# Optimization experiments

Hardware: AMD Instinct MI355X
Metric: run time of the kernel (lower is better)

The kernel has to match this reference:

```python
import jax, jax.numpy as jnp
import numpy as np

B, C_IN, C_OUT, H, W = 128, 128, 128, 40, 40
NUM_EXPERTS, TOP_K, EXPAND = 8, 2, 2
C_HID = C_IN * EXPAND


def setup_inputs() -> dict:
    key = jax.random.key(0)
    ks = jax.random.split(key, 6)
    x = jax.random.normal(ks[0], (B, C_IN, H, W), dtype=jnp.float32)
    weights = jax.random.uniform(ks[1], (B, TOP_K), dtype=jnp.float32)
    indices = jax.random.randint(ks[2], (B, TOP_K), 0, NUM_EXPERTS, dtype=jnp.int64)
    # per-expert 1x1 conv params: expand -> SiLU -> project
    W1 = jax.random.normal(ks[3], (NUM_EXPERTS, C_HID, C_IN), dtype=jnp.float32) * (1.0 / np.sqrt(C_IN))
    b1 = jnp.zeros((NUM_EXPERTS, C_HID), dtype=jnp.float32)
    W2 = jax.random.normal(ks[4], (NUM_EXPERTS, C_OUT, C_HID), dtype=jnp.float32) * (1.0 / np.sqrt(C_HID))
    b2 = jnp.zeros((NUM_EXPERTS, C_OUT), dtype=jnp.float32)
    return {"x": x, "weights": weights, "indices": indices,
            "W1": W1, "b1": b1, "W2": W2, "b2": b2}


def reference(x, weights, indices, W1, b1, W2, b2):
    # Combine top-k gate weights per (batch, expert): duplicate expert picks sum,
    # exactly matching the original's per-expert gather + weighted index_add_.
    Bn = x.shape[0]
    E = W1.shape[0]
    gate = jnp.zeros((Bn, E), dtype=x.dtype).at[jnp.arange(Bn)[:, None], indices].add(weights)  # [B, E]
    out = jnp.zeros((Bn, W2.shape[1]) + x.shape[2:], dtype=x.dtype)
    for e in range(E):  # fixed small expert loop
        h = jax.nn.silu(jnp.einsum('bchw,oc->bohw', x, W1[e]) + b1[e][None, :, None, None])
        y = jnp.einsum('bchw,oc->bohw', h, W2[e]) + b2[e][None, :, None, None]
        out = out + y * gate[:, e][:, None, None, None]
    return out
```

## Files before the change

### kernel.cpp

```cpp
#include <hip/hip_runtime.h>

#define CIN   128
#define CHID  256
#define COUT  128
#define HWPX  1600

typedef __attribute__((ext_vector_type(8))) short bf16x8;
typedef __attribute__((ext_vector_type(4))) float f32x4;

__device__ __forceinline__ unsigned short f2bf(float f) {
  unsigned int u = __builtin_bit_cast(unsigned int, f);
  u += 0x7FFFu + ((u >> 16) & 1u);
  return (unsigned short)(u >> 16);
}
__device__ __forceinline__ unsigned int pack_bf2(float a, float b) {
  return (unsigned int)f2bf(a) | ((unsigned int)f2bf(b) << 16);
}
__device__ __forceinline__ unsigned int silu_gate_pk(float a, float b, float g) {
  const float sa = g * a / (1.0f + __expf(-a));
  const float sb = g * b / (1.0f + __expf(-b));
  return pack_bf2(sa, sb);
}

__global__ __launch_bounds__(256) void convert_w_kernel(
    const float* __restrict__ W1, const float* __restrict__ W2,
    unsigned short* __restrict__ W1b, unsigned short* __restrict__ W2b) {
  const int i   = blockIdx.x * 256 + threadIdx.x;
  const int j   = i & 7;
  const int p   = (i >> 3) & 511;
  const int grp = (i >> 12) & 7;
  const int e   = i >> 15;
  {
    const int r   = p >> 4;
    const int c   = ((p & 15) - r) & 15;
    const int row = r & 15, mt = r >> 4;
    const int ch  = grp * 32 + ((row >> 2) << 3) + (row & 3) + (mt << 2);
    W1b[i] = f2bf(W1[(e * CHID + ch) * CIN + c * 8 + j]);
  }
  {
    const int co = p >> 2;
    const int c  = ((p & 3) - co - (co >> 2)) & 3;
    const int ch = grp * 32 + c * 8 + j;
    W2b[i] = f2bf(W2[(e * COUT + co) * CHID + ch]);
  }
}

__global__ __launch_bounds__(256, 2) void moe_kernel(
    const float* __restrict__ x, const float* __restrict__ wts,
    const int* __restrict__ idx, const unsigned short* __restrict__ W1,
    const float* __restrict__ b1, const unsigned short* __restrict__ W2,
    const float* __restrict__ b2, float* __restrict__ out) {
  __shared__ __align__(16) unsigned short lds[40960];

  const int tid  = threadIdx.x;
  const int wave = tid >> 6;
  const int lane = tid & 63;
  const int q    = lane >> 4;
  const int r16  = lane & 15;

  const int  b     = blockIdx.x / 7;
  const int  t4    = blockIdx.x % 7;
  const int  tile  = t4 * 4 + wave;
  const bool valid = (tile < 25);
  const int  tileC = valid ? tile : 24;
  const int  px0   = tileC * 64;

  unsigned short* xw = &lds[wave * 8192];

  {
    const float* xb = x + (long)b * CIN * HWPX + px0 + lane;
#pragma unroll 4
    for (int c = 0; c < 16; ++c) {
      float v[8];
#pragma unroll
      for (int jj = 0; jj < 8; ++jj) v[jj] = xb[(long)(c * 8 + jj) * HWPX];
      union { bf16x8 w; unsigned int u[4]; } t;
#pragma unroll
      for (int d = 0; d < 4; ++d) t.u[d] = pack_bf2(v[2 * d], v[2 * d + 1]);
      const int slot = (c + lane) & 15;
      *reinterpret_cast<bf16x8*>(&xw[(lane * 16 + slot) * 8]) = t.w;
    }
  }

  const int   e0 = idx[b * 2 + 0], e1 = idx[b * 2 + 1];
  const float g0 = wts[b * 2 + 0], g1 = wts[b * 2 + 1];

  f32x4 accO[8][4];
#pragma unroll
  for (int mt = 0; mt < 8; ++mt)
#pragma unroll
    for (int nt = 0; nt < 4; ++nt) accO[mt][nt] = (f32x4){0.f, 0.f, 0.f, 0.f};

  const uint4* w1g = reinterpret_cast<const uint4*>(W1);
  const uint4* w2g = reinterpret_cast<const uint4*>(W2);
  uint4* ws1 = reinterpret_cast<uint4*>(&lds[32768]);
  uint4* ws2 = reinterpret_cast<uint4*>(&lds[36864]);

  uint4 p1a, p1b, p2a, p2b;
  {
    const long base = (long)e0 * 4096 + tid;
    p1a = w1g[base]; p1b = w1g[base + 256];
    p2a = w2g[base]; p2b = w2g[base + 256];
  }

  for (int gs = 0; gs < 16; ++gs) {
    const int   slot = gs >> 3;
    const int   grp  = gs & 7;
    const int   e    = slot ? e1 : e0;
    const float g    = slot ? g1 : g0;

    __syncthreads();
    ws1[tid] = p1a; ws1[tid + 256] = p1b;
    ws2[tid] = p2a; ws2[tid + 256] = p2b;
    __syncthreads();

    if (gs < 15) {
      const int  gs2  = gs + 1;
      const int  e2   = (gs2 >> 3) ? e1 : e0;
      const long base = (long)e2 * 4096 + (long)(gs2 & 7) * 512 + tid;
      p1a = w1g[base]; p1b = w1g[base + 256];
      p2a = w2g[base]; p2b = w2g[base + 256];
    }

    f32x4 aA[4], aB[4];
#pragma unroll
    for (int nt = 0; nt < 4; ++nt) {
      aA[nt] = (f32x4){0.f, 0.f, 0.f, 0.f};
      aB[nt] = (f32x4){0.f, 0.f, 0.f, 0.f};
    }
#pragma unroll
    for (int ks = 0; ks < 4; ++ks) {
      const int slotw = (ks * 4 + q + r16) & 15;
      const bf16x8 w0 = *reinterpret_cast<const bf16x8*>(
          &lds[32768 + (r16 * 16 + slotw) * 8]);
      const bf16x8 w1v = *reinterpret_cast<const bf16x8*>(
          &lds[32768 + ((r16 + 16) * 16 + slotw) * 8]);
#pragma unroll
      for (int nt = 0; nt < 4; ++nt) {
        const int px = nt * 16 + r16;
        const bf16x8 xf = *reinterpret_cast<const bf16x8*>(
            &xw[(px * 16 + ((ks * 4 + q + px) & 15)) * 8]);
        aA[nt] = __builtin_amdgcn_mfma_f32_16x16x32_bf16(w0, xf, aA[nt], 0, 0, 0);
        aB[nt] = __builtin_amdgcn_mfma_f32_16x16x32_bf16(w1v, xf, aB[nt], 0, 0, 0);
      }
    }

    const float* b1e = b1 + e * CHID + grp * 32;
    const f32x4 bA = *reinterpret_cast<const f32x4*>(&b1e[q * 8]);
    const f32x4 bB = *reinterpret_cast<const f32x4*>(&b1e[q * 8 + 4]);
    union { bf16x8 v; unsigned int u[4]; } h[4];
#pragma unroll
    for (int nt = 0; nt < 4; ++nt) {
      h[nt].u[0] = silu_gate_pk(aA[nt][0] + bA[0], aA[nt][1] + bA[1], g);
      h[nt].u[1] = silu_gate_pk(aA[nt][2] + bA[2], aA[nt][3] + bA[3], g);
      h[nt].u[2] = silu_gate_pk(aB[nt][0] + bB[0], aB[nt][1] + bB[1], g);
      h[nt].u[3] = silu_gate_pk(aB[nt][2] + bB[2], aB[nt][3] + bB[3], g);
    }

#pragma unroll
    for (int mt = 0; mt < 8; ++mt) {
      const int co = mt * 16 + r16;
      const bf16x8 w2v = *reinterpret_cast<const bf16x8*>(
          &lds[36864 + (co * 4 + ((q + co + (co >> 2)) & 3)) * 8]);
#pragma unroll
      for (int nt = 0; nt < 4; ++nt)
        accO[mt][nt] = __builtin_amdgcn_mfma_f32_16x16x32_bf16(w2v, h[nt].v, accO[mt][nt], 0, 0, 0);
    }
  }

  float* eb = reinterpret_cast<float*>(xw);
  const float* b2e0 = b2 + e0 * COUT;
  const float* b2e1 = b2 + e1 * COUT;
  const int  coR   = lane >> 2;
  const int  qtr   = lane & 3;
  const long orow0 = (long)b * COUT * HWPX + px0 + qtr * 16;
#pragma unroll
  for (int mt = 0; mt < 8; ++mt) {
    const int coW = q * 4;
    const f32x4 bias = g0 * (*reinterpret_cast<const f32x4*>(&b2e0[mt * 16 + coW])) +
                       g1 * (*reinterpret_cast<const f32x4*>(&b2e1[mt * 16 + coW]));
#pragma unroll
    for (int nt = 0; nt < 4; ++nt) {
      const f32x4 v = accO[mt][nt] + bias;
#pragma unroll
      for (int rr = 0; rr < 4; ++rr)
        eb[(coW + rr) * 68 + nt * 16 + r16] = v[rr];
    }
    if (valid) {
      const long orow = orow0 + (long)(mt * 16 + coR) * HWPX;
#pragma unroll
      for (int i4 = 0; i4 < 4; ++i4) {
        const float4 ov = *reinterpret_cast<const float4*>(
            &eb[coR * 68 + qtr * 16 + i4 * 4]);
        *reinterpret_cast<float4*>(&out[orow + i4 * 4]) = ov;
      }
    }
  }
}

extern "C" void kernel_launch(void* const* d_in, const int* in_sizes, int n_in,
                              void* d_out, int out_size, void* d_ws, size_t ws_size,
                              hipStream_t stream) {
  const float* x   = (const float*)d_in[0];
  const float* wts = (const float*)d_in[1];
  const int*   idx = (const int*)d_in[2];
  const float* W1  = (const float*)d_in[3];
  const float* b1  = (const float*)d_in[4];
  const float* W2  = (const float*)d_in[5];
  const float* b2  = (const float*)d_in[6];
  float* out = (float*)d_out;

  unsigned short* W1b = (unsigned short*)d_ws;
  unsigned short* W2b = (unsigned short*)d_ws + (8 * CHID * CIN);

  convert_w_kernel<<<262144 / 256, 256, 0, stream>>>(W1, W2, W1b, W2b);
  moe_kernel<<<128 * 7, 256, 0, stream>>>(x, wts, idx, W1b, b1, W2b, b2, out);
}
```

Measured before the change: 302.0 us.

## Load expert weights directly from global in MFMA fragment order, drop LDS staging

The weight conversion kernel now writes bf16 weights pre-swizzled into per-lane MFMA fragment order. Each wave then reads its W1/W2 fragments straight from global memory (L2/L1) instead of staging them through LDS behind two block-wide barriers per step. This removes the __syncthreads pairs and the weight LDS region, which lets idle waves return early. It also switches SiLU to exp2/rcp intrinsics and makes the expert indices wave-uniform. The cost is global/L2 load latency on the MFMA inner loop with no explicit prefetch.

Result: slower. 314.1 us (+4.0%).

```diff
diff --git a/kernel.cpp b/kernel.cpp
--- a/kernel.cpp
+++ b/kernel.cpp
@@ -17,31 +17,36 @@
   return (unsigned int)f2bf(a) | ((unsigned int)f2bf(b) << 16);
 }
 __device__ __forceinline__ unsigned int silu_gate_pk(float a, float b, float g) {
-  const float sa = g * a / (1.0f + __expf(-a));
-  const float sb = g * b / (1.0f + __expf(-b));
+  const float ea = __builtin_amdgcn_exp2f(a * -1.442695041f);
+  const float eb = __builtin_amdgcn_exp2f(b * -1.442695041f);
+  const float sa = g * a * __builtin_amdgcn_rcpf(1.0f + ea);
+  const float sb = g * b * __builtin_amdgcn_rcpf(1.0f + eb);
   return pack_bf2(sa, sb);
 }
 
 __global__ __launch_bounds__(256) void convert_w_kernel(
     const float* __restrict__ W1, const float* __restrict__ W2,
-    unsigned short* __restrict__ W1b, unsigned short* __restrict__ W2b) {
-  const int i   = blockIdx.x * 256 + threadIdx.x;
-  const int j   = i & 7;
-  const int p   = (i >> 3) & 511;
-  const int grp = (i >> 12) & 7;
-  const int e   = i >> 15;
+    unsigned short* __restrict__ W1c, unsigned short* __restrict__ W2c) {
+  const int i    = blockIdx.x * 256 + threadIdx.x;
+  const int j    = i & 7;
+  const int lane = (i >> 3) & 63;
+  const int r16  = lane & 15;
+  const int q    = lane >> 4;
   {
-    const int r   = p >> 4;
-    const int c   = ((p & 15) - r) & 15;
-    const int row = r & 15, mt = r >> 4;
-    const int ch  = grp * 32 + ((row >> 2) << 3) + (row & 3) + (mt << 2);
-    W1b[i] = f2bf(W1[(e * CHID + ch) * CIN + c * 8 + j]);
+    const int half = (i >> 9) & 1;
+    const int ks   = (i >> 10) & 3;
+    const int grp  = (i >> 12) & 7;
+    const int e    = i >> 15;
+    const int ch   = grp * 32 + ((r16 >> 2) << 3) + (r16 & 3) + (half << 2);
+    const int c    = ks * 4 + q;
+    W1c[i] = f2bf(W1[(e * CHID + ch) * CIN + c * 8 + j]);
   }
   {
-    const int co = p >> 2;
-    const int c  = ((p & 3) - co - (co >> 2)) & 3;
-    const int ch = grp * 32 + c * 8 + j;
-    W2b[i] = f2bf(W2[(e * COUT + co) * CHID + ch]);
+    const int mt  = (i >> 9) & 7;
+    const int grp = (i >> 12) & 7;
+    const int e   = i >> 15;
+    const int co  = mt * 16 + r16;
+    W2c[i] = f2bf(W2[(e * COUT + co) * CHID + grp * 32 + q * 8 + j]);
   }
 }
 
@@ -50,7 +55,7 @@
     const int* __restrict__ idx, const unsigned short* __restrict__ W1,
     const float* __restrict__ b1, const unsigned short* __restrict__ W2,
     const float* __restrict__ b2, float* __restrict__ out) {
-  __shared__ __align__(16) unsigned short lds[40960];
+  __shared__ __align__(16) unsigned short lds[32768];
 
   const int tid  = threadIdx.x;
   const int wave = tid >> 6;
@@ -58,12 +63,11 @@
   const int q    = lane >> 4;
   const int r16  = lane & 15;
 
-  const int  b     = blockIdx.x / 7;
-  const int  t4    = blockIdx.x % 7;
-  const int  tile  = t4 * 4 + wave;
-  const bool valid = (tile < 25);
-  const int  tileC = valid ? tile : 24;
-  const int  px0   = tileC * 64;
+  const int  b    = blockIdx.x / 7;
+  const int  t4   = blockIdx.x % 7;
+  const int  tile = t4 * 4 + wave;
+  if (tile >= 25) return;
+  const int  px0  = tile * 64;
 
   unsigned short* xw = &lds[wave * 8192];
 
@@ -82,7 +86,8 @@
     }
   }
 
-  const int   e0 = idx[b * 2 + 0], e1 = idx[b * 2 + 1];
+  const int   e0 = __builtin_amdgcn_readfirstlane(idx[b * 2 + 0]);
+  const int   e1 = __builtin_amdgcn_readfirstlane(idx[b * 2 + 1]);
   const float g0 = wts[b * 2 + 0], g1 = wts[b * 2 + 1];
 
   f32x4 accO[8][4];
@@ -91,36 +96,15 @@
 #pragma unroll
     for (int nt = 0; nt < 4; ++nt) accO[mt][nt] = (f32x4){0.f, 0.f, 0.f, 0.f};
 
-  const uint4* w1g = reinterpret_cast<const uint4*>(W1);
-  const uint4* w2g = reinterpret_cast<const uint4*>(W2);
-  uint4* ws1 = reinterpret_cast<uint4*>(&lds[32768]);
-  uint4* ws2 = reinterpret_cast<uint4*>(&lds[36864]);
-
-  uint4 p1a, p1b, p2a, p2b;
-  {
-    const long base = (long)e0 * 4096 + tid;
-    p1a = w1g[base]; p1b = w1g[base + 256];
-    p2a = w2g[base]; p2b = w2g[base + 256];
-  }
+  const int lane8 = lane * 8;
 
   for (int gs = 0; gs < 16; ++gs) {
     const int   slot = gs >> 3;
     const int   grp  = gs & 7;
     const int   e    = slot ? e1 : e0;
     const float g    = slot ? g1 : g0;
-
-    __syncthreads();
-    ws1[tid] = p1a; ws1[tid + 256] = p1b;
-    ws2[tid] = p2a; ws2[tid + 256] = p2b;
-    __syncthreads();
-
-    if (gs < 15) {
-      const int  gs2  = gs + 1;
-      const int  e2   = (gs2 >> 3) ? e1 : e0;
-      const long base = (long)e2 * 4096 + (long)(gs2 & 7) * 512 + tid;
-      p1a = w1g[base]; p1b = w1g[base + 256];
-      p2a = w2g[base]; p2b = w2g[base + 256];
-    }
+    const unsigned short* w1s = W1 + ((long)(e * 8 + grp) << 12);
+    const unsigned short* w2s = W2 + ((long)(e * 8 + grp) << 12);
 
     f32x4 aA[4], aB[4];
 #pragma unroll
@@ -130,11 +114,10 @@
     }
 #pragma unroll
     for (int ks = 0; ks < 4; ++ks) {
-      const int slotw = (ks * 4 + q + r16) & 15;
       const bf16x8 w0 = *reinterpret_cast<const bf16x8*>(
-          &lds[32768 + (r16 * 16 + slotw) * 8]);
+          &w1s[(ks * 2 + 0) * 512 + lane8]);
       const bf16x8 w1v = *reinterpret_cast<const bf16x8*>(
-          &lds[32768 + ((r16 + 16) * 16 + slotw) * 8]);
+          &w1s[(ks * 2 + 1) * 512 + lane8]);
 #pragma unroll
       for (int nt = 0; nt < 4; ++nt) {
         const int px = nt * 16 + r16;
@@ -159,9 +142,8 @@
 
 #pragma unroll
     for (int mt = 0; mt < 8; ++mt) {
-      const int co = mt * 16 + r16;
       const bf16x8 w2v = *reinterpret_cast<const bf16x8*>(
-          &lds[36864 + (co * 4 + ((q + co + (co >> 2)) & 3)) * 8]);
+          &w2s[mt * 512 + lane8]);
 #pragma unroll
       for (int nt = 0; nt < 4; ++nt)
         accO[mt][nt] = __builtin_amdgcn_mfma_f32_16x16x32_bf16(w2v, h[nt].v, accO[mt][nt], 0, 0, 0);
@@ -186,7 +168,7 @@
       for (int rr = 0; rr < 4; ++rr)
         eb[(coW + rr) * 68 + nt * 16 + r16] = v[rr];
     }
-    if (valid) {
+    {
       const long orow = orow0 + (long)(mt * 16 + coR) * HWPX;
 #pragma unroll
       for (int i4 = 0; i4 < 4; ++i4) {
@@ -210,9 +192,9 @@
   const float* b2  = (const float*)d_in[6];
   float* out = (float*)d_out;
 
-  unsigned short* W1b = (unsigned short*)d_ws;
-  unsigned short* W2b = (unsigned short*)d_ws + (8 * CHID * CIN);
-
-  convert_w_kernel<<<262144 / 256, 256, 0, stream>>>(W1, W2, W1b, W2b);
-  moe_kernel<<<128 * 7, 256, 0, stream>>>(x, wts, idx, W1b, b1, W2b, b2, out);
-}
+  unsigned short* W1c = (unsigned short*)d_ws;
+  unsigned short* W2c = (unsigned short*)d_ws + (8 * CHID * CIN);
+
+  convert_w_kernel<<<262144 / 256, 256, 0, stream>>>(W1, W2, W1c, W2c);
+  moe_kernel<<<128 * 7, 256, 0, stream>>>(x, wts, idx, W1c, b1, W2c, b2, out);
+}
```

## Restructure MoE kernel: 4 blocks per batch, 32px tiles, async double-buffered weights

Applied to the files above, without the earlier changes.

Each batch is now split across 4 blocks instead of 7, and pixel tiles shrink from 64 to 32. Each wave handles 3–4 tiles and keeps accumulators for all of them, so every weight fragment loaded from LDS is reused across more pixels and padded wasted tiles go away. Weights are copied straight from global memory into a double-buffered LDS region with global_load_lds and waited on via vmcnt, replacing the register staging and two barriers per step. SiLU now uses exp2/rcp intrinsics. The cost is a much larger accumulator register footprint (occupancy drops to 1 block) and a grid of 512 blocks that may underfill the GPU.

Result: slower. 316.4 us (+4.7%).

```diff
diff --git a/kernel.cpp b/kernel.cpp
--- a/kernel.cpp
+++ b/kernel.cpp
@@ -4,6 +4,9 @@
 #define CHID  256
 #define COUT  128
 #define HWPX  1600
+#define TPX   32
+#define XOFF  0
+#define WOFF  53248
 
 typedef __attribute__((ext_vector_type(8))) short bf16x8;
 typedef __attribute__((ext_vector_type(4))) float f32x4;
@@ -17,8 +20,10 @@
   return (unsigned int)f2bf(a) | ((unsigned int)f2bf(b) << 16);
 }
 __device__ __forceinline__ unsigned int silu_gate_pk(float a, float b, float g) {
-  const float sa = g * a / (1.0f + __expf(-a));
-  const float sb = g * b / (1.0f + __expf(-b));
+  const float ea = __builtin_amdgcn_exp2f(a * -1.442695041f);
+  const float eb = __builtin_amdgcn_exp2f(b * -1.442695041f);
+  const float sa = g * a * __builtin_amdgcn_rcpf(1.0f + ea);
+  const float sb = g * b * __builtin_amdgcn_rcpf(1.0f + eb);
   return pack_bf2(sa, sb);
 }
 
@@ -45,12 +50,30 @@
   }
 }
 
-__global__ __launch_bounds__(256, 2) void moe_kernel(
+__device__ __forceinline__ void stage_w(const unsigned short* W1b,
+                                        const unsigned short* W2b,
+                                        int e, int grp, unsigned short* wb,
+                                        int wave, int lane) {
+  const long s = ((long)(e * 8 + grp) << 12) + wave * 1024 + lane * 8;
+#pragma unroll
+  for (int k2 = 0; k2 < 2; ++k2) {
+    __builtin_amdgcn_global_load_lds(
+        (const __attribute__((address_space(1))) unsigned int*)(W1b + s + k2 * 512),
+        (__attribute__((address_space(3))) unsigned int*)(wb + wave * 1024 + k2 * 512),
+        16, 0, 0);
+    __builtin_amdgcn_global_load_lds(
+        (const __attribute__((address_space(1))) unsigned int*)(W2b + s + k2 * 512),
+        (__attribute__((address_space(3))) unsigned int*)(wb + 4096 + wave * 1024 + k2 * 512),
+        16, 0, 0);
+  }
+}
+
+__global__ __launch_bounds__(256, 1) void moe_kernel(
     const float* __restrict__ x, const float* __restrict__ wts,
-    const int* __restrict__ idx, const unsigned short* __restrict__ W1,
-    const float* __restrict__ b1, const unsigned short* __restrict__ W2,
+    const int* __restrict__ idx, const unsigned short* __restrict__ W1b,
+    const float* __restrict__ b1, const unsigned short* __restrict__ W2b,
     const float* __restrict__ b2, float* __restrict__ out) {
-  __shared__ __align__(16) unsigned short lds[40960];
+  __shared__ __align__(16) unsigned short lds[69632];
 
   const int tid  = threadIdx.x;
   const int wave = tid >> 6;
@@ -58,141 +81,152 @@
   const int q    = lane >> 4;
   const int r16  = lane & 15;
 
-  const int  b     = blockIdx.x / 7;
-  const int  t4    = blockIdx.x % 7;
-  const int  tile  = t4 * 4 + wave;
-  const bool valid = (tile < 25);
-  const int  tileC = valid ? tile : 24;
-  const int  px0   = tileC * 64;
-
-  unsigned short* xw = &lds[wave * 8192];
+  const int b    = blockIdx.x >> 2;
+  const int blkp = blockIdx.x & 3;
+  const int cnt  = (blkp < 2) ? 13 : 12;
+  const int T0   = blkp * 12 + (blkp < 2 ? blkp : 2);
+  const int ntw  = 3 + ((cnt == 13 && wave == 0) ? 1 : 0);
+  const int ws   = 3 * wave + ((cnt == 13 && wave > 0) ? 1 : 0);
+
+  const int   e0 = __builtin_amdgcn_readfirstlane(idx[b * 2 + 0]);
+  const int   e1 = __builtin_amdgcn_readfirstlane(idx[b * 2 + 1]);
+  const float g0 = wts[b * 2 + 0], g1 = wts[b * 2 + 1];
+
+  stage_w(W1b, W2b, e0, 0, &lds[WOFF + 0 * 8192], wave, lane);
+  stage_w(W1b, W2b, e0, 1, &lds[WOFF + 1 * 8192], wave, lane);
 
   {
-    const float* xb = x + (long)b * CIN * HWPX + px0 + lane;
-#pragma unroll 4
-    for (int c = 0; c < 16; ++c) {
-      float v[8];
-#pragma unroll
-      for (int jj = 0; jj < 8; ++jj) v[jj] = xb[(long)(c * 8 + jj) * HWPX];
-      union { bf16x8 w; unsigned int u[4]; } t;
-#pragma unroll
-      for (int d = 0; d < 4; ++d) t.u[d] = pack_bf2(v[2 * d], v[2 * d + 1]);
-      const int slot = (c + lane) & 15;
-      *reinterpret_cast<bf16x8*>(&xw[(lane * 16 + slot) * 8]) = t.w;
-    }
-  }
-
-  const int   e0 = idx[b * 2 + 0], e1 = idx[b * 2 + 1];
-  const float g0 = wts[b * 2 + 0], g1 = wts[b * 2 + 1];
-
-  f32x4 accO[8][4];
-#pragma unroll
-  for (int mt = 0; mt < 8; ++mt)
-#pragma unroll
-    for (int nt = 0; nt < 4; ++nt) accO[mt][nt] = (f32x4){0.f, 0.f, 0.f, 0.f};
-
-  const uint4* w1g = reinterpret_cast<const uint4*>(W1);
-  const uint4* w2g = reinterpret_cast<const uint4*>(W2);
-  uint4* ws1 = reinterpret_cast<uint4*>(&lds[32768]);
-  uint4* ws2 = reinterpret_cast<uint4*>(&lds[36864]);
-
-  uint4 p1a, p1b, p2a, p2b;
-  {
-    const long base = (long)e0 * 4096 + tid;
-    p1a = w1g[base]; p1b = w1g[base + 256];
-    p2a = w2g[base]; p2b = w2g[base + 256];
-  }
+    const int p = lane & 31, hh = lane >> 5;
+    for (int lt = ws; lt < ws + ntw; ++lt) {
+      const int gt = T0 + lt;
+      const float* xr = x + (long)b * CIN * HWPX + gt * TPX + p;
+      unsigned short* xw = &lds[XOFF + lt * 4096];
+#pragma unroll
+      for (int it = 0; it < 8; ++it) {
+        const int cc = it * 2 + hh;
+        float v[8];
+#pragma unroll
+        for (int jj = 0; jj < 8; ++jj) v[jj] = xr[(long)(cc * 8 + jj) * HWPX];
+        union { bf16x8 w; unsigned int u[4]; } t;
+#pragma unroll
+        for (int d = 0; d < 4; ++d) t.u[d] = pack_bf2(v[2 * d], v[2 * d + 1]);
+        const int slot = (cc + p) & 15;
+        *reinterpret_cast<bf16x8*>(&xw[(p * 16 + slot) * 8]) = t.w;
+      }
+    }
+  }
+
+  f32x4 accO[4][8][2];
+#pragma unroll
+  for (int t = 0; t < 4; ++t)
+#pragma unroll
+    for (int mt = 0; mt < 8; ++mt)
+#pragma unroll
+      for (int nt = 0; nt < 2; ++nt) accO[t][mt][nt] = (f32x4){0.f, 0.f, 0.f, 0.f};
 
   for (int gs = 0; gs < 16; ++gs) {
-    const int   slot = gs >> 3;
-    const int   grp  = gs & 7;
-    const int   e    = slot ? e1 : e0;
-    const float g    = slot ? g1 : g0;
-
-    __syncthreads();
-    ws1[tid] = p1a; ws1[tid + 256] = p1b;
-    ws2[tid] = p2a; ws2[tid + 256] = p2b;
-    __syncthreads();
-
-    if (gs < 15) {
-      const int  gs2  = gs + 1;
-      const int  e2   = (gs2 >> 3) ? e1 : e0;
-      const long base = (long)e2 * 4096 + (long)(gs2 & 7) * 512 + tid;
-      p1a = w1g[base]; p1b = w1g[base + 256];
-      p2a = w2g[base]; p2b = w2g[base + 256];
-    }
-
-    f32x4 aA[4], aB[4];
-#pragma unroll
-    for (int nt = 0; nt < 4; ++nt) {
-      aA[nt] = (f32x4){0.f, 0.f, 0.f, 0.f};
-      aB[nt] = (f32x4){0.f, 0.f, 0.f, 0.f};
-    }
+    const int   sl  = gs >> 3;
+    const int   grp = gs & 7;
+    const int   e   = sl ? e1 : e0;
+    const float g   = sl ? g1 : g0;
+    unsigned short* wb = &lds[WOFF + (gs & 1) * 8192];
+
+    asm volatile("s_waitcnt vmcnt(4)" ::: "memory");
+    __builtin_amdgcn_sched_barrier(0);
+    __builtin_amdgcn_s_barrier();
+
+    bf16x8 w1f[8];
 #pragma unroll
     for (int ks = 0; ks < 4; ++ks) {
       const int slotw = (ks * 4 + q + r16) & 15;
-      const bf16x8 w0 = *reinterpret_cast<const bf16x8*>(
-          &lds[32768 + (r16 * 16 + slotw) * 8]);
-      const bf16x8 w1v = *reinterpret_cast<const bf16x8*>(
-          &lds[32768 + ((r16 + 16) * 16 + slotw) * 8]);
-#pragma unroll
-      for (int nt = 0; nt < 4; ++nt) {
-        const int px = nt * 16 + r16;
-        const bf16x8 xf = *reinterpret_cast<const bf16x8*>(
-            &xw[(px * 16 + ((ks * 4 + q + px) & 15)) * 8]);
-        aA[nt] = __builtin_amdgcn_mfma_f32_16x16x32_bf16(w0, xf, aA[nt], 0, 0, 0);
-        aB[nt] = __builtin_amdgcn_mfma_f32_16x16x32_bf16(w1v, xf, aB[nt], 0, 0, 0);
-      }
-    }
-
+      w1f[ks * 2 + 0] = *reinterpret_cast<const bf16x8*>(&wb[(r16 * 16 + slotw) * 8]);
+      w1f[ks * 2 + 1] = *reinterpret_cast<const bf16x8*>(&wb[((r16 + 16) * 16 + slotw) * 8]);
+    }
+    bf16x8 w2f[8];
+#pragma unroll
+    for (int mt = 0; mt < 8; ++mt) {
+      const int co = mt * 16 + r16;
+      w2f[mt] = *reinterpret_cast<const bf16x8*>(
+          &wb[4096 + (co * 4 + ((q + co + (co >> 2)) & 3)) * 8]);
+    }
     const float* b1e = b1 + e * CHID + grp * 32;
     const f32x4 bA = *reinterpret_cast<const f32x4*>(&b1e[q * 8]);
     const f32x4 bB = *reinterpret_cast<const f32x4*>(&b1e[q * 8 + 4]);
-    union { bf16x8 v; unsigned int u[4]; } h[4];
-#pragma unroll
-    for (int nt = 0; nt < 4; ++nt) {
-      h[nt].u[0] = silu_gate_pk(aA[nt][0] + bA[0], aA[nt][1] + bA[1], g);
-      h[nt].u[1] = silu_gate_pk(aA[nt][2] + bA[2], aA[nt][3] + bA[3], g);
-      h[nt].u[2] = silu_gate_pk(aB[nt][0] + bB[0], aB[nt][1] + bB[1], g);
-      h[nt].u[3] = silu_gate_pk(aB[nt][2] + bB[2], aB[nt][3] + bB[3], g);
-    }
-
-#pragma unroll
-    for (int mt = 0; mt < 8; ++mt) {
-      const int co = mt * 16 + r16;
-      const bf16x8 w2v = *reinterpret_cast<const bf16x8*>(
-          &lds[36864 + (co * 4 + ((q + co + (co >> 2)) & 3)) * 8]);
-#pragma unroll
-      for (int nt = 0; nt < 4; ++nt)
-        accO[mt][nt] = __builtin_amdgcn_mfma_f32_16x16x32_bf16(w2v, h[nt].v, accO[mt][nt], 0, 0, 0);
-    }
-  }
-
-  float* eb = reinterpret_cast<float*>(xw);
+
+#pragma unroll
+    for (int t = 0; t < 4; ++t) {
+      if (t < ntw) {
+        const unsigned short* xw = &lds[XOFF + (ws + t) * 4096];
+        f32x4 aA[2], aB[2];
+#pragma unroll
+        for (int nt = 0; nt < 2; ++nt) {
+          aA[nt] = (f32x4){0.f, 0.f, 0.f, 0.f};
+          aB[nt] = (f32x4){0.f, 0.f, 0.f, 0.f};
+        }
+#pragma unroll
+        for (int ks = 0; ks < 4; ++ks) {
+#pragma unroll
+          for (int nt = 0; nt < 2; ++nt) {
+            const int px = nt * 16 + r16;
+            const bf16x8 xf = *reinterpret_cast<const bf16x8*>(
+                &xw[(px * 16 + ((ks * 4 + q + px) & 15)) * 8]);
+            aA[nt] = __builtin_amdgcn_mfma_f32_16x16x32_bf16(w1f[ks * 2 + 0], xf, aA[nt], 0, 0, 0);
+            aB[nt] = __builtin_amdgcn_mfma_f32_16x16x32_bf16(w1f[ks * 2 + 1], xf, aB[nt], 0, 0, 0);
+          }
+        }
+        union { bf16x8 v; unsigned int u[4]; } h[2];
+#pragma unroll
+        for (int nt = 0; nt < 2; ++nt) {
+          h[nt].u[0] = silu_gate_pk(aA[nt][0] + bA[0], aA[nt][1] + bA[1], g);
+          h[nt].u[1] = silu_gate_pk(aA[nt][2] + bA[2], aA[nt][3] + bA[3], g);
+          h[nt].u[2] = silu_gate_pk(aB[nt][0] + bB[0], aB[nt][1] + bB[1], g);
+          h[nt].u[3] = silu_gate_pk(aB[nt][2] + bB[2], aB[nt][3] + bB[3], g);
+        }
+#pragma unroll
+        for (int mt = 0; mt < 8; ++mt)
+#pragma unroll
+          for (int nt = 0; nt < 2; ++nt)
+            accO[t][mt][nt] = __builtin_amdgcn_mfma_f32_16x16x32_bf16(w2f[mt], h[nt].v, accO[t][mt][nt], 0, 0, 0);
+      }
+    }
+
+    __builtin_amdgcn_s_barrier();
+    if (gs <= 14) {
+      const int gs2  = (gs + 2 <= 15) ? gs + 2 : 15;
+      const int e2   = (gs2 >> 3) ? e1 : e0;
+      stage_w(W1b, W2b, e2, gs2 & 7, wb, wave, lane);
+    }
+  }
+
   const float* b2e0 = b2 + e0 * COUT;
   const float* b2e1 = b2 + e1 * COUT;
-  const int  coR   = lane >> 2;
-  const int  qtr   = lane & 3;
-  const long orow0 = (long)b * COUT * HWPX + px0 + qtr * 16;
-#pragma unroll
-  for (int mt = 0; mt < 8; ++mt) {
-    const int coW = q * 4;
-    const f32x4 bias = g0 * (*reinterpret_cast<const f32x4*>(&b2e0[mt * 16 + coW])) +
-                       g1 * (*reinterpret_cast<const f32x4*>(&b2e1[mt * 16 + coW]));
-#pragma unroll
-    for (int nt = 0; nt < 4; ++nt) {
-      const f32x4 v = accO[mt][nt] + bias;
-#pragma unroll
-      for (int rr = 0; rr < 4; ++rr)
-        eb[(coW + rr) * 68 + nt * 16 + r16] = v[rr];
-    }
-    if (valid) {
-      const long orow = orow0 + (long)(mt * 16 + coR) * HWPX;
-#pragma unroll
-      for (int i4 = 0; i4 < 4; ++i4) {
-        const float4 ov = *reinterpret_cast<const float4*>(
-            &eb[coR * 68 + qtr * 16 + i4 * 4]);
-        *reinterpret_cast<float4*>(&out[orow + i4 * 4]) = ov;
+  const int coR = lane >> 2;
+  const int qtr = lane & 3;
+#pragma unroll
+  for (int t = 0; t < 4; ++t) {
+    if (t < ntw) {
+      float* eb = reinterpret_cast<float*>(&lds[XOFF + (ws + t) * 4096]);
+      const long px0   = (long)(T0 + ws + t) * TPX;
+      const long obase = (long)b * COUT * HWPX + px0;
+#pragma unroll
+      for (int mt = 0; mt < 8; ++mt) {
+        const int coW = q * 4;
+        const f32x4 bias = g0 * (*reinterpret_cast<const f32x4*>(&b2e0[mt * 16 + coW])) +
+                           g1 * (*reinterpret_cast<const f32x4*>(&b2e1[mt * 16 + coW]));
+#pragma unroll
+        for (int nt = 0; nt < 2; ++nt) {
+          const f32x4 v = accO[t][mt][nt] + bias;
+#pragma unroll
+          for (int rr = 0; rr < 4; ++rr)
+            eb[(coW + rr) * 36 + nt * 16 + r16] = v[rr];
+        }
+        const long orow = obase + (long)(mt * 16 + coR) * HWPX;
+#pragma unroll
+        for (int k = 0; k < 2; ++k) {
+          const float4 ov = *reinterpret_cast<const float4*>(
+              &eb[coR * 36 + k * 16 + qtr * 4]);
+          *reinterpret_cast<float4*>(&out[orow + k * 16 + qtr * 4]) = ov;
+        }
       }
     }
   }
@@ -214,5 +248,5 @@
   unsigned short* W2b = (unsigned short*)d_ws + (8 * CHID * CIN);
 
   convert_w_kernel<<<262144 / 256, 256, 0, stream>>>(W1, W2, W1b, W2b);
-  moe_kernel<<<128 * 7, 256, 0, stream>>>(x, wts, idx, W1b, b1, W2b, b2, out);
-}
+  moe_kernel<<<128 * 4, 256, 0, stream>>>(x, wts, idx, W1b, b1, W2b, b2, out);
+}
```
